# Performance work log

Measured on AMD Instinct MI355X. Metric: run time of the kernel, lower is better.

Reference implementation:

```python
import jax, jax.numpy as jnp
import numpy as np

DIM = 2048
NUM_EXPERTS = 8
N_TOKENS = 8192
SPARSITY = 0.8  # sparsity_constraint parameter (used only to derive static k)
K = max(1, int(SPARSITY * NUM_EXPERTS))  # = 6


def setup_inputs() -> dict:
    key = jax.random.key(0)
    ks = jax.random.split(key, 5)
    scale = 1.0 / np.sqrt(DIM)
    x = jax.random.normal(ks[0], (N_TOKENS, DIM), dtype=jnp.float32)
    Wg = jax.random.uniform(ks[1], (NUM_EXPERTS, DIM), jnp.float32, -scale, scale)
    bg = jax.random.uniform(ks[2], (NUM_EXPERTS,), jnp.float32, -scale, scale)
    We = jax.random.uniform(ks[3], (NUM_EXPERTS, DIM, DIM), jnp.float32, -scale, scale)
    be = jax.random.uniform(ks[4], (NUM_EXPERTS, DIM), jnp.float32, -scale, scale)
    return {"x": x, "Wg": Wg, "bg": bg, "We": We, "be": be}


def reference(x, Wg, bg, We, be):
    # gate scores: [N, E]
    gate_scores = x @ Wg.T + bg
    # top-k expert indices per token: [N, K]
    _, topk_idx = jax.lax.top_k(gate_scores, K)
    # mask[n, e] = expert e is among token n's top-k: [N, E]
    mask = jnp.any(topk_idx[:, :, None] == jnp.arange(NUM_EXPERTS)[None, None, :], axis=1)
    # all expert outputs: [N, E, D]  (We is [E, out, in]; Linear = x @ W.T + b)
    expert_out = jnp.einsum('nd,efd->nef', x, We) + be[None, :, :]
    # combine: unweighted sum of selected experts' outputs (no gate weighting in source)
    out = jnp.sum(expert_out * mask[:, :, None].astype(x.dtype), axis=1)
    return out
```

## Files before the change

### kernel.cpp

```cpp
#include <hip/hip_runtime.h>
#include <hip/hip_bf16.h>
#include <stdint.h>

#define DIM 2048
#define NEXP 8
#define NTOK 8192
#define KSEL 6
#define NPAIR 28
#define SLOTS 92

typedef short bf16x8 __attribute__((ext_vector_type(8)));
typedef float f32x4 __attribute__((ext_vector_type(4)));
typedef const __attribute__((address_space(1))) unsigned int GU32;
typedef __attribute__((address_space(3))) unsigned int LU32;

static constexpr int PA[NPAIR] = {0,0,0,0,0,0,0,1,1,1,1,1,1,2,2,2,2,2,3,3,3,3,4,4,4,5,5,6};
static constexpr int PB[NPAIR] = {1,2,3,4,5,6,7,2,3,4,5,6,7,3,4,5,6,7,4,5,6,7,5,6,7,6,7,7};

__device__ __forceinline__ unsigned short f2b(float f) {
  union { float f; uint32_t u; } v; v.f = f;
  return (unsigned short)((v.u + 0x7fffu + ((v.u >> 16) & 1u)) >> 16);
}

__global__ void zero_cnt_kernel(int* cnt) {
  if (threadIdx.x < NPAIR) cnt[threadIdx.x] = 0;
}

__global__ __launch_bounds__(256) void gate_kernel(
    const float* __restrict__ x, const float* __restrict__ Wg,
    const float* __restrict__ bg, unsigned short* __restrict__ xB,
    int* __restrict__ pid) {
  int t = threadIdx.x;
  int w = t >> 6, l = t & 63;
  int n = blockIdx.x * 4 + w;
  const float* xr = x + (size_t)n * DIM;
  float xv[32];
#pragma unroll
  for (int j = 0; j < 8; ++j) {
    float4 v = *(const float4*)(xr + 4 * l + 256 * j);
    xv[4 * j + 0] = v.x; xv[4 * j + 1] = v.y;
    xv[4 * j + 2] = v.z; xv[4 * j + 3] = v.w;
  }
  unsigned short* xbr = xB + (size_t)n * DIM;
#pragma unroll
  for (int j = 0; j < 8; ++j) {
    ushort4 o;
    o.x = f2b(xv[4 * j + 0]); o.y = f2b(xv[4 * j + 1]);
    o.z = f2b(xv[4 * j + 2]); o.w = f2b(xv[4 * j + 3]);
    *(ushort4*)(xbr + 4 * l + 256 * j) = o;
  }
  float sc[NEXP];
#pragma unroll
  for (int e = 0; e < NEXP; ++e) {
    const float* wr = Wg + e * DIM;
    float s = 0.f;
#pragma unroll
    for (int j = 0; j < 8; ++j) {
      float4 v = *(const float4*)(wr + 4 * l + 256 * j);
      s += xv[4 * j + 0] * v.x + xv[4 * j + 1] * v.y +
           xv[4 * j + 2] * v.z + xv[4 * j + 3] * v.w;
    }
#pragma unroll
    for (int off = 32; off > 0; off >>= 1) s += __shfl_xor(s, off, 64);
    sc[e] = s + bg[e];
  }
  if (l == 0) {
    int ex0 = -1, ex1 = -1;
#pragma unroll
    for (int e = 0; e < NEXP; ++e) {
      int rank = 0;
#pragma unroll
      for (int j = 0; j < NEXP; ++j)
        rank += (sc[j] > sc[e]) || (sc[j] == sc[e] && j < e);
      if (rank >= KSEL) { if (ex0 < 0) ex0 = e; else if (ex1 < 0) ex1 = e; }
    }
    pid[n] = ex0 * (15 - ex0) / 2 + (ex1 - ex0 - 1);
  }
}

__global__ __launch_bounds__(256) void bucket_kernel(
    const int* __restrict__ pid, int* __restrict__ cnt, int* __restrict__ list) {
  __shared__ int lcnt[NPAIR];
  __shared__ int gbase[NPAIR];
  int t = threadIdx.x;
  if (t < NPAIR) lcnt[t] = 0;
  __syncthreads();
  int base = blockIdx.x * 2048;
  int p[8], lp[8];
#pragma unroll
  for (int j = 0; j < 8; ++j) {
    int n = base + t + 256 * j;
    p[j] = pid[n];
    lp[j] = atomicAdd(&lcnt[p[j]], 1);
  }
  __syncthreads();
  if (t < NPAIR) gbase[t] = atomicAdd(&cnt[t], lcnt[t]);
  __syncthreads();
#pragma unroll
  for (int j = 0; j < 8; ++j) {
    int n = base + t + 256 * j;
    list[p[j] * NTOK + gbase[p[j]] + lp[j]] = n;
  }
}

__global__ void tilemap_kernel(const int* __restrict__ cnt, int* __restrict__ tileBase) {
  if (threadIdx.x == 0) {
    int s = 0;
    for (int p = 0; p < NPAIR; ++p) { tileBase[p] = s; s += (cnt[p] + 127) >> 7; }
    tileBase[NPAIR] = s;
  }
}

__global__ __launch_bounds__(256) void biaspair_kernel(
    const float* __restrict__ be, float* __restrict__ biasPair) {
  int f = blockIdx.x * 256 + threadIdx.x;
  float v[NEXP]; float s = 0.f;
#pragma unroll
  for (int e = 0; e < NEXP; ++e) { v[e] = be[e * DIM + f]; s += v[e]; }
#pragma unroll
  for (int pp = 0; pp < NPAIR; ++pp)
    biasPair[pp * DIM + f] = s - v[PA[pp]] - v[PB[pp]];
}

__global__ __launch_bounds__(256) void pairw_kernel(
    const float* __restrict__ We, unsigned short* __restrict__ Wp,
    int fbase, int frows) {
  size_t pos = ((size_t)blockIdx.x * 256 + threadIdx.x) * 4;
  size_t src = (size_t)fbase * DIM + pos;
  float4 v[NEXP];
  float sx = 0.f, sy = 0.f, sz = 0.f, sw = 0.f;
#pragma unroll
  for (int e = 0; e < NEXP; ++e) {
    v[e] = *(const float4*)(We + (size_t)e * DIM * DIM + src);
    sx += v[e].x; sy += v[e].y; sz += v[e].z; sw += v[e].w;
  }
  size_t chunk = (size_t)frows * DIM;
#pragma unroll
  for (int pp = 0; pp < NPAIR; ++pp) {
    int a = PA[pp], b = PB[pp];
    ushort4 o;
    o.x = f2b(sx - v[a].x - v[b].x);
    o.y = f2b(sy - v[a].y - v[b].y);
    o.z = f2b(sz - v[a].z - v[b].z);
    o.w = f2b(sw - v[a].w - v[b].w);
    *(ushort4*)(Wp + (size_t)pp * chunk + pos) = o;
  }
}

__global__ __launch_bounds__(256, 3) void gemm_pair(
    const unsigned short* __restrict__ A, const unsigned short* __restrict__ Wp,
    const int* __restrict__ cnt, const int* __restrict__ list,
    const int* __restrict__ tileBase, const float* __restrict__ biasPair,
    float* __restrict__ out, int fbase, int frows) {
  __shared__ unsigned short sA[128 * 64];
  __shared__ unsigned short sB[128 * 64];
  __shared__ int sRows[128];
  int slot = blockIdx.y, ft = blockIdx.x;
  if (slot >= tileBase[NPAIR]) return;
  int p = 0;
  while (p + 1 < NPAIR && tileBase[p + 1] <= slot) ++p;
  int c = cnt[p];
  int m0 = (slot - tileBase[p]) * 128;

  int t = threadIdx.x;
  int w = t >> 6, l = t & 63;
  int wm = w & 1, wn = w >> 1;
  int quad = l >> 4, lr = l & 15;
  int cs = (l & 7) ^ ((l >> 3) & 7);

  if (t < 128) {
    int idx = m0 + t;
    if (idx >= c) idx = c - 1;
    sRows[t] = list[p * NTOK + idx];
  }
  __syncthreads();

  size_t rowOffA[4], rowOffB[4];
#pragma unroll
  for (int i = 0; i < 4; ++i)
    rowOffA[i] = (size_t)sRows[i * 32 + w * 8 + (l >> 3)] * DIM;
  const unsigned short* Bb =
      Wp + (size_t)p * frows * DIM + (size_t)ft * 128 * DIM;
#pragma unroll
  for (int i = 0; i < 4; ++i)
    rowOffB[i] = (size_t)(i * 32 + w * 8 + (l >> 3)) * DIM;

  f32x4 acc[4][4];
#pragma unroll
  for (int mi = 0; mi < 4; ++mi)
#pragma unroll
    for (int ni = 0; ni < 4; ++ni) {
      acc[mi][ni][0] = 0.f; acc[mi][ni][1] = 0.f;
      acc[mi][ni][2] = 0.f; acc[mi][ni][3] = 0.f;
    }

  for (int k0 = 0; k0 < DIM; k0 += 64) {
#pragma unroll
    for (int i = 0; i < 4; ++i) {
      __builtin_amdgcn_global_load_lds((GU32*)(A + rowOffA[i] + k0 + cs * 8),
          (LU32*)(sA + (i * 32 + w * 8) * 64), 16, 0, 0);
      __builtin_amdgcn_global_load_lds((GU32*)(Bb + rowOffB[i] + k0 + cs * 8),
          (LU32*)(sB + (i * 32 + w * 8) * 64), 16, 0, 0);
    }
    __syncthreads();
#pragma unroll
    for (int ks = 0; ks < 2; ++ks) {
      bf16x8 aF[4], bF[4];
#pragma unroll
      for (int mi = 0; mi < 4; ++mi)
        aF[mi] = *(const bf16x8*)(sA + (wm * 64 + mi * 16 + lr) * 64 +
                                  (((ks << 2) | quad) ^ (lr & 7)) * 8);
#pragma unroll
      for (int ni = 0; ni < 4; ++ni)
        bF[ni] = *(const bf16x8*)(sB + (wn * 64 + ni * 16 + lr) * 64 +
                                  (((ks << 2) | quad) ^ (lr & 7)) * 8);
#pragma unroll
      for (int mi = 0; mi < 4; ++mi)
#pragma unroll
        for (int ni = 0; ni < 4; ++ni)
          acc[mi][ni] = __builtin_amdgcn_mfma_f32_16x16x32_bf16(aF[mi], bF[ni], acc[mi][ni], 0, 0, 0);
    }
    __syncthreads();
  }

  int f0 = fbase + ft * 128;
  float bb[4];
#pragma unroll
  for (int ni = 0; ni < 4; ++ni)
    bb[ni] = biasPair[p * DIM + f0 + wn * 64 + ni * 16 + lr];
#pragma unroll
  for (int mi = 0; mi < 4; ++mi) {
#pragma unroll
    for (int i = 0; i < 4; ++i) {
      int lrow = wm * 64 + mi * 16 + quad * 4 + i;
      if (m0 + lrow < c) {
        float* orow = out + (size_t)sRows[lrow] * DIM + f0;
#pragma unroll
        for (int ni = 0; ni < 4; ++ni)
          orow[wn * 64 + ni * 16 + lr] = acc[mi][ni][i] + bb[ni];
      }
    }
  }
}

extern "C" void kernel_launch(void* const* d_in, const int* in_sizes, int n_in,
                              void* d_out, int out_size, void* d_ws, size_t ws_size,
                              hipStream_t stream) {
  const float* x  = (const float*)d_in[0];
  const float* Wg = (const float*)d_in[1];
  const float* bg = (const float*)d_in[2];
  const float* We = (const float*)d_in[3];
  const float* be = (const float*)d_in[4];
  float* out = (float*)d_out;

  char* ws = (char*)d_ws;
  unsigned short* xB = (unsigned short*)ws; ws += (size_t)NTOK * DIM * 2;
  int* pid = (int*)ws;          ws += (size_t)NTOK * 4;
  int* cnt = (int*)ws;          ws += 128;
  int* tileBase = (int*)ws;     ws += 128;
  int* list = (int*)ws;         ws += (size_t)NPAIR * NTOK * 4;
  float* biasPair = (float*)ws; ws += (size_t)NPAIR * DIM * 4;
  unsigned short* Wp = (unsigned short*)ws;

  size_t avail = ws_size - (size_t)(ws - (char*)d_ws);
  int NR = 1;
  while (NR < 16 && (size_t)NPAIR * DIM * (size_t)(DIM / NR) * 2 > avail) NR <<= 1;
  int frows = DIM / NR;

  zero_cnt_kernel<<<1, 64, 0, stream>>>(cnt);
  gate_kernel<<<NTOK / 4, 256, 0, stream>>>(x, Wg, bg, xB, pid);
  bucket_kernel<<<4, 256, 0, stream>>>(pid, cnt, list);
  tilemap_kernel<<<1, 64, 0, stream>>>(cnt, tileBase);
  biaspair_kernel<<<DIM / 256, 256, 0, stream>>>(be, biasPair);
  for (int r = 0; r < NR; ++r) {
    int fbase = r * frows;
    pairw_kernel<<<(frows * DIM) / 1024, 256, 0, stream>>>(We, Wp, fbase, frows);
    gemm_pair<<<dim3(frows / 128, SLOTS), 256, 0, stream>>>(
        xB, Wp, cnt, list, tileBase, biasPair, out, fbase, frows);
  }
}
```

Before: 464.3 us.

## Merge bucketing kernels, widen pair-weight stores, raise gemm occupancy, reverse slot order

Replaces the zero, bucket and tilemap kernels with a single one-block kernel that counts, sets tile bases and fills the token lists, which removes two launches. The pair-weight builder now handles 8 elements per thread with 16-byte stores. The GEMM launch bound rises to 4 blocks per CU, and slots are processed in reverse order so the partial tail tiles are scheduled first. An unused, broken bucket_all kernel is left in the file, and the single-block bucketing serialises that step.

```diff
diff --git a/kernel.cpp b/kernel.cpp
--- a/kernel.cpp
+++ b/kernel.cpp
@@ -10,6 +10,7 @@
 #define SLOTS 92
 
 typedef short bf16x8 __attribute__((ext_vector_type(8)));
+typedef unsigned short u16x8 __attribute__((ext_vector_type(8)));
 typedef float f32x4 __attribute__((ext_vector_type(4)));
 typedef const __attribute__((address_space(1))) unsigned int GU32;
 typedef __attribute__((address_space(3))) unsigned int LU32;
@@ -20,10 +21,6 @@
 __device__ __forceinline__ unsigned short f2b(float f) {
   union { float f; uint32_t u; } v; v.f = f;
   return (unsigned short)((v.u + 0x7fffu + ((v.u >> 16) & 1u)) >> 16);
-}
-
-__global__ void zero_cnt_kernel(int* cnt) {
-  if (threadIdx.x < NPAIR) cnt[threadIdx.x] = 0;
 }
 
 __global__ __launch_bounds__(256) void gate_kernel(
@@ -78,36 +75,67 @@
   }
 }
 
-__global__ __launch_bounds__(256) void bucket_kernel(
-    const int* __restrict__ pid, int* __restrict__ cnt, int* __restrict__ list) {
+__global__ __launch_bounds__(1024) void bucket_all(
+    const int* __restrict__ pid, int* __restrict__ cnt,
+    int* __restrict__ tileBase, int* __restrict__ list) {
   __shared__ int lcnt[NPAIR];
-  __shared__ int gbase[NPAIR];
+  __shared__ int lpos[NPAIR];
+  __shared__ int lbase[NPAIR];
   int t = threadIdx.x;
-  if (t < NPAIR) lcnt[t] = 0;
-  __syncthreads();
-  int base = blockIdx.x * 2048;
-  int p[8], lp[8];
-#pragma unroll
-  for (int j = 0; j < 8; ++j) {
-    int n = base + t + 256 * j;
-    p[j] = pid[n];
-    lp[j] = atomicAdd(&lcnt[p[j]], 1);
-  }
-  __syncthreads();
-  if (t < NPAIR) gbase[t] = atomicAdd(&cnt[t], lcnt[t]);
-  __syncthreads();
-#pragma unroll
-  for (int j = 0; j < 8; ++j) {
-    int n = base + t + 256 * j;
-    list[p[j] * NTOK + gbase[p[j]] + lp[j]] = n;
-  }
-}
-
-__global__ void tilemap_kernel(const int* __restrict__ cnt, int* __restrict__ tileBase) {
-  if (threadIdx.x == 0) {
-    int s = 0;
-    for (int p = 0; p < NPAIR; ++p) { tileBase[p] = s; s += (cnt[p] + 127) >> 7; }
-    tileBase[NPAIR] = s;
+  if (t < NPAIR) { lcnt[t] = 0; lpos[t] = 0; }
+  __syncthreads();
+  int p[8];
+#pragma unroll
+  for (int j = 0; j < 8; ++j) {
+    p[j] = pid[t + 1024 * j];
+    atomicAdd(&lcnt[p[j]], 1);
+  }
+  __syncthreads();
+  if (t == 0) {
+    int s = 0, ts = 0;
+    for (int q = 0; q < NPAIR; ++q) {
+      lbase[q] = s; s += lcnt[q];
+      cnt[q] = lcnt[q];
+      tileBase[q] = ts; ts += (lcnt[q] + 127) >> 7;
+    }
+    tileBase[NPAIR] = ts;
+  }
+  __syncthreads();
+#pragma unroll
+  for (int j = 0; j < 8; ++j) {
+    int pos = atomicAdd(&lpos[p[j]], 1);
+    list[p[j] * NTOK + lbase[p[j]] + pos - lbase[p[j]] + 0] = 0;
+  }
+}
+
+__global__ __launch_bounds__(1024) void bucket_all2(
+    const int* __restrict__ pid, int* __restrict__ cnt,
+    int* __restrict__ tileBase, int* __restrict__ list) {
+  __shared__ int lcnt[NPAIR];
+  __shared__ int lpos[NPAIR];
+  int t = threadIdx.x;
+  if (t < NPAIR) { lcnt[t] = 0; lpos[t] = 0; }
+  __syncthreads();
+  int p[8];
+#pragma unroll
+  for (int j = 0; j < 8; ++j) {
+    p[j] = pid[t + 1024 * j];
+    atomicAdd(&lcnt[p[j]], 1);
+  }
+  __syncthreads();
+  if (t == 0) {
+    int ts = 0;
+    for (int q = 0; q < NPAIR; ++q) {
+      cnt[q] = lcnt[q];
+      tileBase[q] = ts; ts += (lcnt[q] + 127) >> 7;
+    }
+    tileBase[NPAIR] = ts;
+  }
+  __syncthreads();
+#pragma unroll
+  for (int j = 0; j < 8; ++j) {
+    int pos = atomicAdd(&lpos[p[j]], 1);
+    list[p[j] * NTOK + pos] = t + 1024 * j;
   }
 }
 
@@ -125,29 +153,33 @@
 __global__ __launch_bounds__(256) void pairw_kernel(
     const float* __restrict__ We, unsigned short* __restrict__ Wp,
     int fbase, int frows) {
-  size_t pos = ((size_t)blockIdx.x * 256 + threadIdx.x) * 4;
+  size_t pos = ((size_t)blockIdx.x * 256 + threadIdx.x) * 8;
   size_t src = (size_t)fbase * DIM + pos;
-  float4 v[NEXP];
-  float sx = 0.f, sy = 0.f, sz = 0.f, sw = 0.f;
+  float v[NEXP][8];
+  float s[8];
+#pragma unroll
+  for (int i = 0; i < 8; ++i) s[i] = 0.f;
 #pragma unroll
   for (int e = 0; e < NEXP; ++e) {
-    v[e] = *(const float4*)(We + (size_t)e * DIM * DIM + src);
-    sx += v[e].x; sy += v[e].y; sz += v[e].z; sw += v[e].w;
+    float4 v0 = *(const float4*)(We + (size_t)e * DIM * DIM + src);
+    float4 v1 = *(const float4*)(We + (size_t)e * DIM * DIM + src + 4);
+    v[e][0] = v0.x; v[e][1] = v0.y; v[e][2] = v0.z; v[e][3] = v0.w;
+    v[e][4] = v1.x; v[e][5] = v1.y; v[e][6] = v1.z; v[e][7] = v1.w;
+#pragma unroll
+    for (int i = 0; i < 8; ++i) s[i] += v[e][i];
   }
   size_t chunk = (size_t)frows * DIM;
 #pragma unroll
   for (int pp = 0; pp < NPAIR; ++pp) {
     int a = PA[pp], b = PB[pp];
-    ushort4 o;
-    o.x = f2b(sx - v[a].x - v[b].x);
-    o.y = f2b(sy - v[a].y - v[b].y);
-    o.z = f2b(sz - v[a].z - v[b].z);
-    o.w = f2b(sw - v[a].w - v[b].w);
-    *(ushort4*)(Wp + (size_t)pp * chunk + pos) = o;
-  }
-}
-
-__global__ __launch_bounds__(256, 3) void gemm_pair(
+    u16x8 o;
+#pragma unroll
+    for (int i = 0; i < 8; ++i) o[i] = f2b(s[i] - v[a][i] - v[b][i]);
+    *(u16x8*)(Wp + (size_t)pp * chunk + pos) = o;
+  }
+}
+
+__global__ __launch_bounds__(256, 4) void gemm_pair(
     const unsigned short* __restrict__ A, const unsigned short* __restrict__ Wp,
     const int* __restrict__ cnt, const int* __restrict__ list,
     const int* __restrict__ tileBase, const float* __restrict__ biasPair,
@@ -155,8 +187,10 @@
   __shared__ unsigned short sA[128 * 64];
   __shared__ unsigned short sB[128 * 64];
   __shared__ int sRows[128];
-  int slot = blockIdx.y, ft = blockIdx.x;
-  if (slot >= tileBase[NPAIR]) return;
+  int total = tileBase[NPAIR];
+  if (blockIdx.y >= total) return;
+  int slot = total - 1 - blockIdx.y;
+  int ft = blockIdx.x;
   int p = 0;
   while (p + 1 < NPAIR && tileBase[p + 1] <= slot) ++p;
   int c = cnt[p];
@@ -267,14 +301,12 @@
   while (NR < 16 && (size_t)NPAIR * DIM * (size_t)(DIM / NR) * 2 > avail) NR <<= 1;
   int frows = DIM / NR;
 
-  zero_cnt_kernel<<<1, 64, 0, stream>>>(cnt);
   gate_kernel<<<NTOK / 4, 256, 0, stream>>>(x, Wg, bg, xB, pid);
-  bucket_kernel<<<4, 256, 0, stream>>>(pid, cnt, list);
-  tilemap_kernel<<<1, 64, 0, stream>>>(cnt, tileBase);
+  bucket_all2<<<1, 1024, 0, stream>>>(pid, cnt, tileBase, list);
   biaspair_kernel<<<DIM / 256, 256, 0, stream>>>(be, biasPair);
   for (int r = 0; r < NR; ++r) {
     int fbase = r * frows;
-    pairw_kernel<<<(frows * DIM) / 1024, 256, 0, stream>>>(We, Wp, fbase, frows);
+    pairw_kernel<<<(frows * DIM) / 2048, 256, 0, stream>>>(We, Wp, fbase, frows);
     gemm_pair<<<dim3(frows / 128, SLOTS), 256, 0, stream>>>(
         xB, Wp, cnt, list, tileBase, biasPair, out, fbase, frows);
   }
```

Result: no change. 471.5 us (+1.5%).
